# Performance work log

Hardware: AMD Instinct MI355X
Metric: run time of the kernel (lower is better)

The kernel has to match this reference:

```python
import jax, jax.numpy as jnp
import numpy as np

P = 4          # patch_size
LAM = 0.5      # init_lambda
B, C, H, W = 8, 96, 128, 128

def _dct_mat(N):
    # torch_dct unnormalized DCT-II matrix: D[k,n] = 2*cos(pi*(2n+1)k/(2N))
    n = np.arange(N)
    return 2.0 * np.cos(np.pi * (2.0 * n[None, :] + 1.0) * n[:, None] / (2.0 * N))

_D = jnp.asarray(_dct_mat(P), dtype=jnp.float32)
_Di = jnp.asarray(np.linalg.inv(_dct_mat(P)), dtype=jnp.float32)  # exact inverse -> idct(dct(x)) == x

def _dct2(x):
    # DCT-II over last two dims of [..., P, P]
    return jnp.einsum('ij,...jk,lk->...il', _D, x, _D)

def _idct2(x):
    return jnp.einsum('ij,...jk,lk->...il', _Di, x, _Di)

def _conv3x3(x, w, b):
    y = jax.lax.conv_general_dilated(x, w, (1, 1), 'SAME',
                                     dimension_numbers=('NCHW', 'OIHW', 'NCHW'))
    return y + b[None, :, None, None]

def setup_inputs() -> dict:
    key = jax.random.key(0)
    ks = jax.random.split(key, 5)
    std = 1.0 / np.sqrt(C * 9)
    return {
        'input1': jax.random.normal(ks[0], (B, C, H, W), jnp.float32),
        'input2': jax.random.normal(ks[1], (B, C, H, W), jnp.float32),
        'wq': jax.random.normal(ks[2], (C, C, 3, 3), jnp.float32) * std,
        'bq': jnp.zeros((C,), jnp.float32),
        'wk': jax.random.normal(ks[3], (C, C, 3, 3), jnp.float32) * std,
        'bk': jnp.zeros((C,), jnp.float32),
        'wv': jax.random.normal(ks[4], (C, C, 3, 3), jnp.float32) * std,
        'bv': jnp.zeros((C,), jnp.float32),
        'temperature': jnp.ones((1, 1), jnp.float32),
    }

def reference(input1, input2, wq, bq, wk, bk, wv, bv, temperature):
    b, c, h, w = input1.shape
    F_Q = _conv3x3(input1, wq, bq)
    F_K = _conv3x3(input1, wk, bk)
    F_V = _conv3x3(input2, wv, bv)
    hp, wp = h // P, w // P
    # 'b c (h p1) (w p2) -> b c h w p1 p2'
    to_patch = lambda x: x.reshape(b, c, hp, P, wp, P).transpose(0, 1, 2, 4, 3, 5)
    fft_Q = _dct2(to_patch(F_Q))          # [b,c,hp,wp,P,P]
    fft_K = _dct2(to_patch(F_K))
    F1 = jnp.matmul(fft_Q, fft_K)         # per-patch PxP matmul
    L = hp * wp * P * P                   # == h*w
    F1f = F1.reshape(b, c, L)
    Fq = fft_Q.reshape(b, c, L)
    Fk = fft_K.reshape(b, c, L)
    # channel-channel attention: [b,c,L] @ [b,L,c] -> [b,c,c]
    attn = jnp.einsum('bil,bjl->bij', Fq, Fk) * temperature[0, 0]
    attn = jax.nn.softmax(attn, axis=-1)
    Fcfr = jnp.einsum('bij,bjl->bil', attn, F1f).reshape(b, c, hp, wp, P, P)
    Fcfr_out = _idct2(Fcfr)
    # 'b c h w p1 p2 -> b c (h p1) (w p2)'
    Fcfrout = Fcfr_out.transpose(0, 1, 2, 4, 3, 5).reshape(b, c, h, w)
    out1 = jnp.matmul(Fcfrout, F_V)       # batched HxW matmul (H==W)
    Fdfr = F_V - out1 * LAM
    return jnp.matmul(Fcfrout, F_Q) + Fdfr
```

## Files before the change

kernel.cpp:

```cpp
#include <hip/hip_runtime.h>

typedef unsigned short u16;
typedef unsigned int u32;
typedef __bf16 bf16x8 __attribute__((ext_vector_type(8)));
typedef float f32x4 __attribute__((ext_vector_type(4)));
typedef int i32x4 __attribute__((ext_vector_type(4)));

#define BATCH 8
#define CH 96
#define HWSZ 16384
#define PADP (130*130*96)
#define LSTR 68

#define OFF_FQ     0ULL
#define OFF_FK     50331648ULL
#define OFF_GT     50331648ULL
#define OFF_FVN    75497472ULL
#define OFF_PAD1H  100663296ULL
#define OFF_F1W    100663296ULL
#define OFF_PART   126621696ULL
#define OFF_PAD1L  126621696ULL
#define OFF_PAD2   152580096ULL
#define OFF_FCFR   152580096ULL
#define OFF_FVB    178538496ULL
#define OFF_ATTNB  203704320ULL
#define OFF_WQK    203851776ULL
#define OFF_WV     204515328ULL
#define WS_NEED    204681216ULL

__device__ __forceinline__ u16 f2bf(float f) {
    u32 u = __builtin_bit_cast(u32, f);
    u += 0x7fffu + ((u >> 16) & 1u);
    return (u16)(u >> 16);
}
__device__ __forceinline__ float bf2f(u16 h) {
    u32 u = ((u32)h) << 16;
    return __builtin_bit_cast(float, u);
}
__device__ __forceinline__ f32x4 mfma16(i32x4 a, i32x4 b, f32x4 c) {
    return __builtin_amdgcn_mfma_f32_16x16x32_bf16(
        __builtin_bit_cast(bf16x8, a), __builtin_bit_cast(bf16x8, b), c, 0, 0, 0);
}
__device__ __forceinline__ void gl_lds16(const u16* g, u16* l) {
    __builtin_amdgcn_global_load_lds(
        (const __attribute__((address_space(1))) unsigned int*)g,
        (__attribute__((address_space(3))) unsigned int*)l, 16, 0, 0);
}

__global__ __launch_bounds__(256) void k_diag(float* __restrict__ out, int n, float val) {
    for (int i = blockIdx.x * 256 + threadIdx.x; i < n; i += gridDim.x * 256) out[i] = val;
}

__global__ __launch_bounds__(256) void k_trans2(const float* __restrict__ in1,
        const float* __restrict__ in2, u16* __restrict__ p1h, u16* __restrict__ p1l,
        u16* __restrict__ p2) {
    __shared__ float tile[96][129];
    int which = blockIdx.x >> 10;
    int blk = blockIdx.x & 1023;
    const float* src = which ? in2 : in1;
    u16* dh = which ? p2 : p1h;
    u16* dl = which ? nullptr : p1l;
    int b = blk >> 7, y = blk & 127;
    const float* s = src + (size_t)b * CH * HWSZ + (size_t)y * 128;
    for (int idx = threadIdx.x; idx < CH * 128; idx += 256) {
        int c = idx >> 7, x = idx & 127;
        tile[c][x] = s[(size_t)c * HWSZ + x];
    }
    size_t obase = ((size_t)(b * 130 + y + 1) * 130 + 1) * 96;
    for (int c = threadIdx.x; c < 96; c += 256) {
        dh[obase - 96 + c] = 0;
        dh[obase + 128 * 96 + c] = 0;
        if (dl) { dl[obase - 96 + c] = 0; dl[obase + 128 * 96 + c] = 0; }
    }
    if (y == 0 || y == 127) {
        size_t rb = ((size_t)(b * 130 + (y == 0 ? 0 : 129))) * 130 * 96;
        for (int i = threadIdx.x; i < 130 * 96; i += 256) {
            dh[rb + i] = 0;
            if (dl) dl[rb + i] = 0;
        }
    }
    __syncthreads();
    for (int idx = threadIdx.x; idx < 128 * CH; idx += 256) {
        int x = idx / CH, c = idx - x * CH;
        float v = tile[c][x];
        u16 h = f2bf(v);
        dh[obase + idx] = h;
        if (dl) dl[obase + idx] = f2bf(v - bf2f(h));
    }
}

__global__ __launch_bounds__(128) void k_weights_all(const float* __restrict__ wq,
        const float* __restrict__ wk, const float* __restrict__ wv,
        u16* __restrict__ dqk, u16* __restrict__ dv) {
    int co = blockIdx.x;
    if (co < 192) {
        const float* w = (co < 96) ? wq : wk;
        int cs = (co < 96) ? co : co - 96;
        for (int idx = threadIdx.x; idx < 864; idx += 128) {
            int tap = idx / 96, ci = idx - tap * 96;
            int cic = ci >> 5, g = (ci >> 3) & 3, c7 = ci & 7;
            float v = w[((size_t)cs * 96 + ci) * 9 + tap];
            u16 h = f2bf(v), lo = f2bf(v - bf2f(h));
            size_t s = (size_t)(cic * 9 + tap);
            dqk[(((s * 2 + 0) * 4 + g) * 192 + co) * 8 + c7] = h;
            dqk[(((s * 2 + 1) * 4 + g) * 192 + co) * 8 + c7] = lo;
        }
    } else {
        int cs = co - 192;
        for (int idx = threadIdx.x; idx < 864; idx += 128) {
            int tap = idx / 96, ci = idx - tap * 96;
            int cic = ci >> 5, g = (ci >> 3) & 3, c7 = ci & 7;
            float v = wv[((size_t)cs * 96 + ci) * 9 + tap];
            size_t s = (size_t)(cic * 9 + tap);
            dv[((s * 4 + g) * 96 + cs) * 8 + c7] = f2bf(v);
        }
    }
}

__global__ __launch_bounds__(512, 4) void k_convqk6(
        const u16* __restrict__ ph, const u16* __restrict__ pl,
        const u16* __restrict__ wqk,
        const float* __restrict__ bq, const float* __restrict__ bk,
        float* __restrict__ fq, float* __restrict__ fk) {
    __shared__ u16 wbuf[2][12288];
    const int tid = threadIdx.x;
    const int wg = ((blockIdx.x & 7) << 7) | (blockIdx.x >> 3);
    const int b = wg >> 7, y = wg & 127;
    const int w = tid >> 6, lane = tid & 63, l15 = lane & 15, g = lane >> 4;
    const int wx = w & 3, wc = w >> 2;
    f32x4 acc[2][6];
#pragma unroll
    for (int mf = 0; mf < 2; mf++)
#pragma unroll
        for (int f = 0; f < 6; f++) acc[mf][f] = (f32x4){0.f, 0.f, 0.f, 0.f};
    {
#pragma unroll
        for (int j = 0; j < 3; j++)
            gl_lds16(wqk + (size_t)(tid + j * 512) * 8, &wbuf[0][(size_t)(tid + j * 512) * 8]);
    }
    i32x4 ah0, ah1, al0, al1;
    {
        size_t ab = ((size_t)(b * 130 + y) * 130 + (wx * 32 + l15)) * 96 + g * 8;
        ah0 = *(const i32x4*)(ph + ab);
        ah1 = *(const i32x4*)(ph + ab + 16 * 96);
        al0 = *(const i32x4*)(pl + ab);
        al1 = *(const i32x4*)(pl + ab + 16 * 96);
    }
    __syncthreads();
    for (int s = 0; s < 27; s++) {
        const int cur = s & 1;
        i32x4 nh0, nh1, nl0, nl1;
        if (s + 1 < 27) {
            const u16* src = wqk + (size_t)(s + 1) * 12288;
#pragma unroll
            for (int j = 0; j < 3; j++)
                gl_lds16(src + (size_t)(tid + j * 512) * 8, &wbuf[cur ^ 1][(size_t)(tid + j * 512) * 8]);
            const int s1 = s + 1;
            const int cic1 = s1 / 9, tap1 = s1 - cic1 * 9;
            const int dy1 = tap1 / 3 - 1, dx1 = tap1 - (tap1 / 3) * 3 - 1;
            size_t ab = ((size_t)(b * 130 + y + 1 + dy1) * 130 + (wx * 32 + l15 + 1 + dx1)) * 96
                      + cic1 * 32 + g * 8;
            nh0 = *(const i32x4*)(ph + ab);
            nh1 = *(const i32x4*)(ph + ab + 16 * 96);
            nl0 = *(const i32x4*)(pl + ab);
            nl1 = *(const i32x4*)(pl + ab + 16 * 96);
        }
#pragma unroll
        for (int f = 0; f < 6; f++) {
            const int cob = wc * 96 + f * 16 + l15;
            i32x4 bh = *(const i32x4*)(&wbuf[cur][((0 + g) * 192 + cob) * 8]);
            i32x4 bl = *(const i32x4*)(&wbuf[cur][((4 + g) * 192 + cob) * 8]);
            acc[0][f] = mfma16(ah0, bh, acc[0][f]);
            acc[0][f] = mfma16(ah0, bl, acc[0][f]);
            acc[0][f] = mfma16(al0, bh, acc[0][f]);
            acc[1][f] = mfma16(ah1, bh, acc[1][f]);
            acc[1][f] = mfma16(ah1, bl, acc[1][f]);
            acc[1][f] = mfma16(al1, bh, acc[1][f]);
        }
        __syncthreads();
        if (s + 1 < 27) { ah0 = nh0; ah1 = nh1; al0 = nl0; al1 = nl1; }
    }
    const float* bias = wc ? bk : bq;
    float* op = wc ? fk : fq;
#pragma unroll
    for (int f = 0; f < 6; f++) {
        const int co = f * 16 + l15;
        const float bb = bias[co];
#pragma unroll
        for (int mf = 0; mf < 2; mf++) {
            const int xp = wx * 32 + mf * 16 + g * 4;
#pragma unroll
            for (int r = 0; r < 4; r++)
                op[((size_t)((b * 128 + y) * 128 + xp + r)) * 96 + co] = acc[mf][f][r] + bb;
        }
    }
}

__global__ __launch_bounds__(512, 4) void k_convv7(
        const u16* __restrict__ p2, const u16* __restrict__ wv,
        const float* __restrict__ bv, u16* __restrict__ fvb) {
    __shared__ u16 vbuf[2][9216];
    const int tid = threadIdx.x;
    const int wg = ((blockIdx.x & 7) << 7) | (blockIdx.x >> 3);
    const int b = wg >> 7, y = wg & 127;
    const int w = tid >> 6, lane = tid & 63, l15 = lane & 15, g = lane >> 4;
    const int wx = w & 3, wc = w >> 2;
    f32x4 acc[2][3];
#pragma unroll
    for (int mf = 0; mf < 2; mf++)
#pragma unroll
        for (int f = 0; f < 3; f++) acc[mf][f] = (f32x4){0.f, 0.f, 0.f, 0.f};
    {
        gl_lds16(wv + (size_t)tid * 8, &vbuf[0][(size_t)tid * 8]);
        gl_lds16(wv + (size_t)(512 + tid) * 8, &vbuf[0][(size_t)(512 + tid) * 8]);
        if (tid < 128)
            gl_lds16(wv + (size_t)(1024 + tid) * 8, &vbuf[0][(size_t)(1024 + tid) * 8]);
    }
    i32x4 ah0, ah1;
    {
        size_t ab = ((size_t)(b * 130 + y) * 130 + (wx * 32 + l15)) * 96 + g * 8;
        ah0 = *(const i32x4*)(p2 + ab);
        ah1 = *(const i32x4*)(p2 + ab + 16 * 96);
    }
    __syncthreads();
    for (int gp = 0; gp < 9; gp++) {
        const int cur = gp & 1;
        if (gp + 1 < 9) {
            const u16* src = wv + (size_t)(gp + 1) * 9216;
            gl_lds16(src + (size_t)tid * 8, &vbuf[cur ^ 1][(size_t)tid * 8]);
            gl_lds16(src + (size_t)(512 + tid) * 8, &vbuf[cur ^ 1][(size_t)(512 + tid) * 8]);
            if (tid < 128)
                gl_lds16(src + (size_t)(1024 + tid) * 8, &vbuf[cur ^ 1][(size_t)(1024 + tid) * 8]);
        }
#pragma unroll
        for (int t = 0; t < 3; t++) {
            const int s = gp * 3 + t;
            i32x4 nh0, nh1;
            if (s + 1 < 27) {
                const int s1 = s + 1;
                const int cic1 = s1 / 9, tap1 = s1 - cic1 * 9;
                const int dy1 = tap1 / 3 - 1, dx1 = tap1 - (tap1 / 3) * 3 - 1;
                size_t ab = ((size_t)(b * 130 + y + 1 + dy1) * 130 + (wx * 32 + l15 + 1 + dx1)) * 96
                          + cic1 * 32 + g * 8;
                nh0 = *(const i32x4*)(p2 + ab);
                nh1 = *(const i32x4*)(p2 + ab + 16 * 96);
            }
#pragma unroll
            for (int f = 0; f < 3; f++) {
                const int cof = wc * 48 + f * 16 + l15;
                i32x4 bfr = *(const i32x4*)(&vbuf[cur][(size_t)t * 3072 + (g * 96 + cof) * 8]);
                acc[0][f] = mfma16(ah0, bfr, acc[0][f]);
                acc[1][f] = mfma16(ah1, bfr, acc[1][f]);
            }
            if (s + 1 < 27) { ah0 = nh0; ah1 = nh1; }
        }
        __syncthreads();
    }
#pragma unroll
    for (int f = 0; f < 3; f++) {
        const int co = wc * 48 + f * 16 + l15;
        const float bb = bv[co];
#pragma unroll
        for (int mf = 0; mf < 2; mf++) {
            const int xp = wx * 32 + mf * 16 + g * 4;
#pragma unroll
            for (int r = 0; r < 4; r++)
                fvb[((size_t)((b * 128 + y) * 128 + xp + r)) * 96 + co] = f2bf(acc[mf][f][r] + bb);
        }
    }
}

__global__ __launch_bounds__(256) void k_pattn2(
        const float* __restrict__ fq, const float* __restrict__ fk,
        u16* __restrict__ f1w, float* __restrict__ part) {
    __shared__ __attribute__((aligned(16))) float qs[96 * LSTR];
    __shared__ __attribute__((aligned(16))) float ks[96 * LSTR];
    int wg = ((blockIdx.x & 7) << 7) | (blockIdx.x >> 3);
    int b = wg >> 7, ys = (wg >> 2) & 31, xq = wg & 3;
    int y0 = ys * 4, x0 = xq * 32;
    int tx = threadIdx.x & 15, ty = threadIdx.x >> 4;
    double accD[6][6];
#pragma unroll
    for (int a = 0; a < 6; a++)
#pragma unroll
        for (int bb = 0; bb < 6; bb++) accD[a][bb] = 0.0;
#pragma unroll
    for (int cx = 0; cx < 2; cx++) {
        for (int idx = threadIdx.x; idx < 1536; idx += 256) {
            int p = idx / 24, c0 = (idx - p * 24) * 4;
            int ry = p >> 4, rx = p & 15;
            size_t off = ((size_t)((b * 128 + y0 + ry) * 128 + x0 + cx * 16 + rx)) * 96 + c0;
            f32x4 qv = *(const f32x4*)(fq + off);
            f32x4 kv = *(const f32x4*)(fk + off);
#pragma unroll
            for (int u = 0; u < 4; u++) {
                qs[(c0 + u) * LSTR + p] = qv[u];
                ks[(c0 + u) * LSTR + p] = kv[u];
            }
        }
        __syncthreads();
        for (int item = threadIdx.x; item < 384; item += 256) {
            int j = item / 96, c = item - j * 96;
            f32x4 A[4], Bm[4];
#pragma unroll
            for (int r = 0; r < 4; r++) {
                A[r]  = *(const f32x4*)&qs[c * LSTR + r * 16 + j * 4];
                Bm[r] = *(const f32x4*)&ks[c * LSTR + r * 16 + j * 4];
            }
            float rsB[4], csB[4], rsA[4], tot = 0.f;
#pragma unroll
            for (int r = 0; r < 4; r++) {
                rsB[r] = Bm[r][0] + Bm[r][1] + Bm[r][2] + Bm[r][3];
                rsA[r] = A[r][0] + A[r][1] + A[r][2] + A[r][3];
                tot += rsB[r];
            }
#pragma unroll
            for (int m = 0; m < 4; m++) csB[m] = Bm[0][m] + Bm[1][m] + Bm[2][m] + Bm[3][m];
#pragma unroll
            for (int r = 0; r < 4; r++) {
#pragma unroll
                for (int m = 0; m < 4; m++) {
                    float ab = A[r][0] * Bm[0][m] + A[r][1] * Bm[1][m]
                             + A[r][2] * Bm[2][m] + A[r][3] * Bm[3][m];
                    f1w[((size_t)((b * 128 + y0 + r) * 128 + x0 + cx * 16 + j * 4 + m)) * 96 + c]
                        = f2bf(8.f * ab + 2.f * rsA[r] * csB[m]);
                }
                f32x4 kt;
#pragma unroll
                for (int m = 0; m < 4; m++)
                    kt[m] = 64.f * Bm[r][m] + 16.f * (rsB[r] + csB[m]) + 4.f * tot;
                *(f32x4*)&ks[c * LSTR + r * 16 + j * 4] = kt;
            }
        }
        __syncthreads();
        float acc[6][6];
#pragma unroll
        for (int a = 0; a < 6; a++)
#pragma unroll
            for (int bb = 0; bb < 6; bb++) acc[a][bb] = 0.f;
        for (int l4 = 0; l4 < 16; l4++) {
            f32x4 qv4[6], kv4[6];
#pragma unroll
            for (int a = 0; a < 6; a++)
                qv4[a] = *(const f32x4*)&qs[(ty + 16 * a) * LSTR + l4 * 4];
#pragma unroll
            for (int bb = 0; bb < 6; bb++)
                kv4[bb] = *(const f32x4*)&ks[(tx + 16 * bb) * LSTR + l4 * 4];
#pragma unroll
            for (int a = 0; a < 6; a++)
#pragma unroll
                for (int bb = 0; bb < 6; bb++) {
                    acc[a][bb] += qv4[a][0] * kv4[bb][0];
                    acc[a][bb] += qv4[a][1] * kv4[bb][1];
                    acc[a][bb] += qv4[a][2] * kv4[bb][2];
                    acc[a][bb] += qv4[a][3] * kv4[bb][3];
                }
        }
#pragma unroll
        for (int a = 0; a < 6; a++)
#pragma unroll
            for (int bb = 0; bb < 6; bb++) accD[a][bb] += (double)acc[a][bb];
        __syncthreads();
    }
    int s128 = ys * 4 + xq;
#pragma unroll
    for (int a = 0; a < 6; a++)
#pragma unroll
        for (int bb = 0; bb < 6; bb++)
            part[((size_t)((b * 128 + s128) * 96 + ty + 16 * a)) * 96 + tx + 16 * bb]
                = (float)accD[a][bb];
}

__global__ __launch_bounds__(128) void k_softmax(
        const float* __restrict__ part, const float* __restrict__ temp,
        u16* __restrict__ attnb) {
    __shared__ float red[128];
    int b = blockIdx.x / 96, i2 = blockIdx.x - b * 96;
    int j2 = threadIdx.x;
    float v = 0.f;
    if (j2 < 96) {
        double vd = 0.0;
        for (int s = 0; s < 128; s++)
            vd += (double)part[((size_t)((b * 128 + s) * 96 + i2)) * 96 + j2];
        v = (float)vd * temp[0];
    }
    red[j2] = (j2 < 96) ? v : -3.4e38f;
    __syncthreads();
    for (int off = 64; off >= 1; off >>= 1) {
        if (j2 < off) red[j2] = fmaxf(red[j2], red[j2 + off]);
        __syncthreads();
    }
    float mx = red[0];
    __syncthreads();
    float e = (j2 < 96) ? expf(v - mx) : 0.f;
    red[j2] = e;
    __syncthreads();
    for (int off = 64; off >= 1; off >>= 1) {
        if (j2 < off) red[j2] += red[j2 + off];
        __syncthreads();
    }
    float sum = red[0];
    if (j2 < 96) attnb[((size_t)(b * 96) + i2) * 96 + j2] = f2bf(e / sum);
}

__global__ __launch_bounds__(256) void k_gprep(
        const float* __restrict__ fqn, const u16* __restrict__ fvb,
        u16* __restrict__ gt, u16* __restrict__ fvn) {
    __shared__ u16 lg[8 * 32 * 33];
    __shared__ u16 lv[8 * 32 * 33];
    int blk = blockIdx.x;
    int b = blk / 192;
    int r = blk - b * 192;
    int yt = r / 48; r -= yt * 48;
    int xt = r / 12; int cc = r - xt * 12;
    int y0 = yt * 32, x0 = xt * 32, c0 = cc * 8;
    for (int idx = threadIdx.x; idx < 8192; idx += 256) {
        int pix = idx >> 3, cl = idx & 7;
        int yy = pix >> 5, xx = pix & 31;
        size_t off = ((size_t)((b * 128 + y0 + yy) * 128 + x0 + xx)) * 96 + c0 + cl;
        float q = fqn[off];
        float v = bf2f(fvb[off]);
        int la = (cl * 32 + yy) * 33 + xx;
        lg[la] = f2bf(q - 0.5f * v);
        lv[la] = f2bf(v);
    }
    __syncthreads();
    for (int idx = threadIdx.x; idx < 8192; idx += 256) {
        int yy = idx & 31, xl = (idx >> 5) & 31, cl = idx >> 10;
        gt[((size_t)((b * 96 + c0 + cl) * 128 + x0 + xl)) * 128 + y0 + yy] = lg[(cl * 32 + yy) * 33 + xl];
    }
    for (int idx = threadIdx.x; idx < 8192; idx += 256) {
        int xx = idx & 31, yl = (idx >> 5) & 31, cl = idx >> 10;
        fvn[((size_t)((b * 96 + c0 + cl) * 128 + y0 + yl)) * 128 + x0 + xx] = lv[(cl * 32 + yl) * 33 + xx];
    }
}

__global__ __launch_bounds__(256) void k_fcfr2(
        const u16* __restrict__ attnb, const u16* __restrict__ f1w,
        u16* __restrict__ fc) {
    int b = blockIdx.x >> 6, pc = blockIdx.x & 63;
    int lane = threadIdx.x & 63, wv_ = threadIdx.x >> 6;
    int l15 = lane & 15, g = lane >> 4;
    int pbase = pc * 256 + wv_ * 64;
    f32x4 acc[6][4];
#pragma unroll
    for (int m = 0; m < 6; m++)
#pragma unroll
        for (int n = 0; n < 4; n++) acc[m][n] = (f32x4){0.f, 0.f, 0.f, 0.f};
#pragma unroll
    for (int ks = 0; ks < 3; ks++) {
        int k0 = ks * 32 + g * 8;
        i32x4 afr[6];
#pragma unroll
        for (int m = 0; m < 6; m++)
            afr[m] = *(const i32x4*)(attnb + ((size_t)(b * 96 + m * 16 + l15)) * 96 + k0);
#pragma unroll
        for (int n = 0; n < 4; n++) {
            i32x4 bfr = *(const i32x4*)(f1w + ((size_t)(b * 16384 + pbase + n * 16 + l15)) * 96 + k0);
#pragma unroll
            for (int m = 0; m < 6; m++)
                acc[m][n] = mfma16(afr[m], bfr, acc[m][n]);
        }
    }
#pragma unroll
    for (int m = 0; m < 6; m++)
#pragma unroll
        for (int n = 0; n < 4; n++)
#pragma unroll
            for (int r = 0; r < 4; r++) {
                int i2 = m * 16 + g * 4 + r;
                int pix = pbase + n * 16 + l15;
                fc[((size_t)(b * 96 + i2)) * HWSZ + pix] = f2bf(acc[m][n][r]);
            }
}

__global__ __launch_bounds__(256) void k_final(
        const u16* __restrict__ fc, const u16* __restrict__ gt,
        const u16* __restrict__ fvn, float* __restrict__ out) {
    int b = blockIdx.x / 96, c = blockIdx.x - b * 96;
    int lane = threadIdx.x & 63, wv_ = threadIdx.x >> 6;
    int l15 = lane & 15, g = lane >> 4;
    const u16* A = fc + ((size_t)(b * 96 + c)) * HWSZ;
    const u16* Bm = gt + ((size_t)(b * 96 + c)) * HWSZ;
    f32x4 acc[2][8];
#pragma unroll
    for (int mf = 0; mf < 2; mf++)
#pragma unroll
        for (int nf = 0; nf < 8; nf++) acc[mf][nf] = (f32x4){0.f, 0.f, 0.f, 0.f};
#pragma unroll
    for (int kc = 0; kc < 4; kc++) {
        int k0 = kc * 32 + g * 8;
        i32x4 af[2];
#pragma unroll
        for (int mf = 0; mf < 2; mf++)
            af[mf] = *(const i32x4*)(A + (size_t)(wv_ * 32 + mf * 16 + l15) * 128 + k0);
#pragma unroll
        for (int nf = 0; nf < 8; nf++) {
            i32x4 bf = *(const i32x4*)(Bm + (size_t)(nf * 16 + l15) * 128 + k0);
#pragma unroll
            for (int mf = 0; mf < 2; mf++)
                acc[mf][nf] = mfma16(af[mf], bf, acc[mf][nf]);
        }
    }
    const u16* V = fvn + ((size_t)(b * 96 + c)) * HWSZ;
    float* O = out + ((size_t)(b * 96 + c)) * HWSZ;
#pragma unroll
    for (int mf = 0; mf < 2; mf++)
#pragma unroll
        for (int nf = 0; nf < 8; nf++)
#pragma unroll
            for (int r = 0; r < 4; r++) {
                int y = wv_ * 32 + mf * 16 + g * 4 + r;
                int x = nf * 16 + l15;
                O[y * 128 + x] = acc[mf][nf][r] + bf2f(V[y * 128 + x]);
            }
}

extern "C" void kernel_launch(void* const* d_in, const int* in_sizes, int n_in,
                              void* d_out, int out_size, void* d_ws, size_t ws_size,
                              hipStream_t stream) {
    (void)in_sizes; (void)n_in;
    if (ws_size < (size_t)WS_NEED) {
        k_diag<<<2048, 256, 0, stream>>>((float*)d_out, out_size, (float)(ws_size >> 10));
        return;
    }
    const float* in1 = (const float*)d_in[0];
    const float* in2 = (const float*)d_in[1];
    const float* wq  = (const float*)d_in[2];
    const float* bq  = (const float*)d_in[3];
    const float* wk  = (const float*)d_in[4];
    const float* bk  = (const float*)d_in[5];
    const float* wv  = (const float*)d_in[6];
    const float* bv  = (const float*)d_in[7];
    const float* temp = (const float*)d_in[8];
    char* ws = (char*)d_ws;
    float* FQ   = (float*)(ws + OFF_FQ);
    float* FK   = (float*)(ws + OFF_FK);
    u16*  GT    = (u16*)(ws + OFF_GT);
    u16*  FVN   = (u16*)(ws + OFF_FVN);
    u16*  PAD1H = (u16*)(ws + OFF_PAD1H);
    u16*  PAD1L = (u16*)(ws + OFF_PAD1L);
    u16*  PAD2  = (u16*)(ws + OFF_PAD2);
    u16*  F1W   = (u16*)(ws + OFF_F1W);
    float* PART = (float*)(ws + OFF_PART);
    u16*  FCFR  = (u16*)(ws + OFF_FCFR);
    u16*  FVB   = (u16*)(ws + OFF_FVB);
    u16*  ATTNB = (u16*)(ws + OFF_ATTNB);
    u16*  WQK   = (u16*)(ws + OFF_WQK);
    u16*  WV    = (u16*)(ws + OFF_WV);

    k_trans2<<<2048, 256, 0, stream>>>(in1, in2, PAD1H, PAD1L, PAD2);
    k_weights_all<<<288, 128, 0, stream>>>(wq, wk, wv, WQK, WV);
    k_convqk6<<<1024, 512, 0, stream>>>(PAD1H, PAD1L, WQK, bq, bk, FQ, FK);
    k_convv7<<<1024, 512, 0, stream>>>(PAD2, WV, bv, FVB);
    k_pattn2<<<1024, 256, 0, stream>>>(FQ, FK, F1W, PART);
    k_softmax<<<768, 128, 0, stream>>>(PART, temp, ATTNB);
    k_gprep<<<1536, 256, 0, stream>>>(FQ, FVB, GT, FVN);
    k_fcfr2<<<512, 256, 0, stream>>>(ATTNB, F1W, FCFR);
    k_final<<<768, 256, 0, stream>>>(FCFR, GT, FVN, (float*)d_out);
}
```

Before: 367.2 us.

## Write conv outputs in NCHW layout and drop FV transpose in gprep

The Q/K/V conv kernels now write their outputs in planar NCHW layout with vectorized stores, instead of pixel-major NHWC. This lets the patch-attention loader read contiguous rows and store float4s straight to LDS. The gprep kernel no longer has to transpose and write FVN, since conv V emits it directly. The change affects the store pattern of the conv kernels, which may now be less coalesced per wave, and it leaves a dead computation in convv7p.

```diff
diff --git a/kernel.cpp b/kernel.cpp
--- a/kernel.cpp
+++ b/kernel.cpp
@@ -5,6 +5,7 @@
 typedef __bf16 bf16x8 __attribute__((ext_vector_type(8)));
 typedef float f32x4 __attribute__((ext_vector_type(4)));
 typedef int i32x4 __attribute__((ext_vector_type(4)));
+typedef unsigned int u32x2 __attribute__((ext_vector_type(2)));
 
 #define BATCH 8
 #define CH 96
@@ -15,14 +16,13 @@
 #define OFF_FQ     0ULL
 #define OFF_FK     50331648ULL
 #define OFF_GT     50331648ULL
-#define OFF_FVN    75497472ULL
 #define OFF_PAD1H  100663296ULL
 #define OFF_F1W    100663296ULL
 #define OFF_PART   126621696ULL
 #define OFF_PAD1L  126621696ULL
 #define OFF_PAD2   152580096ULL
 #define OFF_FCFR   152580096ULL
-#define OFF_FVB    178538496ULL
+#define OFF_FVN    178538496ULL
 #define OFF_ATTNB  203704320ULL
 #define OFF_WQK    203851776ULL
 #define OFF_WV     204515328ULL
@@ -117,7 +117,7 @@
     }
 }
 
-__global__ __launch_bounds__(512, 4) void k_convqk6(
+__global__ __launch_bounds__(512, 4) void k_convqk6p(
         const u16* __restrict__ ph, const u16* __restrict__ pl,
         const u16* __restrict__ wqk,
         const float* __restrict__ bq, const float* __restrict__ bk,
@@ -189,16 +189,17 @@
 #pragma unroll
         for (int mf = 0; mf < 2; mf++) {
             const int xp = wx * 32 + mf * 16 + g * 4;
-#pragma unroll
-            for (int r = 0; r < 4; r++)
-                op[((size_t)((b * 128 + y) * 128 + xp + r)) * 96 + co] = acc[mf][f][r] + bb;
-        }
-    }
-}
-
-__global__ __launch_bounds__(512, 4) void k_convv7(
+            f32x4 o;
+#pragma unroll
+            for (int r = 0; r < 4; r++) o[r] = acc[mf][f][r] + bb;
+            *(f32x4*)(op + ((size_t)((b * 96 + co) * 128 + y)) * 128 + xp) = o;
+        }
+    }
+}
+
+__global__ __launch_bounds__(512, 4) void k_convv7p(
         const u16* __restrict__ p2, const u16* __restrict__ wv,
-        const float* __restrict__ bv, u16* __restrict__ fvb) {
+        const float* __restrict__ bv, u16* __restrict__ fvn) {
     __shared__ u16 vbuf[2][9216];
     const int tid = threadIdx.x;
     const int wg = ((blockIdx.x & 7) << 7) | (blockIdx.x >> 3);
@@ -263,14 +264,19 @@
 #pragma unroll
         for (int mf = 0; mf < 2; mf++) {
             const int xp = wx * 32 + mf * 16 + g * 4;
-#pragma unroll
-            for (int r = 0; r < 4; r++)
-                fvb[((size_t)((b * 128 + y) * 128 + xp + r)) * 96 + co] = f2bf(acc[mf][f][r] + bb);
-        }
-    }
-}
-
-__global__ __launch_bounds__(256) void k_pattn2(
+            u32 lo = (u32)f2bf(acc[mf][f][0]) | ((u32)f2bf(acc[mf][f][1] + bb - bb + bb) << 16);
+            u16 o0 = f2bf(acc[mf][f][0] + bb), o1 = f2bf(acc[mf][f][1] + bb);
+            u16 o2 = f2bf(acc[mf][f][2] + bb), o3 = f2bf(acc[mf][f][3] + bb);
+            u32x2 pk;
+            pk[0] = (u32)o0 | ((u32)o1 << 16);
+            pk[1] = (u32)o2 | ((u32)o3 << 16);
+            (void)lo;
+            *(u32x2*)(fvn + ((size_t)((b * 96 + co) * 128 + y)) * 128 + xp) = pk;
+        }
+    }
+}
+
+__global__ __launch_bounds__(256) void k_pattn2p(
         const float* __restrict__ fq, const float* __restrict__ fk,
         u16* __restrict__ f1w, float* __restrict__ part) {
     __shared__ __attribute__((aligned(16))) float qs[96 * LSTR];
@@ -287,16 +293,13 @@
 #pragma unroll
     for (int cx = 0; cx < 2; cx++) {
         for (int idx = threadIdx.x; idx < 1536; idx += 256) {
-            int p = idx / 24, c0 = (idx - p * 24) * 4;
-            int ry = p >> 4, rx = p & 15;
-            size_t off = ((size_t)((b * 128 + y0 + ry) * 128 + x0 + cx * 16 + rx)) * 96 + c0;
+            int c = idx >> 4, rem = idx & 15, ry = rem >> 2, q4 = rem & 3;
+            size_t off = ((size_t)((b * 96 + c) * 128 + y0 + ry)) * 128 + x0 + cx * 16 + q4 * 4;
             f32x4 qv = *(const f32x4*)(fq + off);
             f32x4 kv = *(const f32x4*)(fk + off);
-#pragma unroll
-            for (int u = 0; u < 4; u++) {
-                qs[(c0 + u) * LSTR + p] = qv[u];
-                ks[(c0 + u) * LSTR + p] = kv[u];
-            }
+            int p0 = ry * 16 + q4 * 4;
+            *(f32x4*)&qs[c * LSTR + p0] = qv;
+            *(f32x4*)&ks[c * LSTR + p0] = kv;
         }
         __syncthreads();
         for (int item = threadIdx.x; item < 384; item += 256) {
@@ -369,6 +372,34 @@
         for (int bb = 0; bb < 6; bb++)
             part[((size_t)((b * 128 + s128) * 96 + ty + 16 * a)) * 96 + tx + 16 * bb]
                 = (float)accD[a][bb];
+}
+
+__global__ __launch_bounds__(256) void k_gprep2(
+        const float* __restrict__ fqp, const u16* __restrict__ fvn,
+        u16* __restrict__ gt) {
+    __shared__ u16 lg[8 * 32 * 33];
+    int blk = blockIdx.x;
+    int b = blk / 192;
+    int r = blk - b * 192;
+    int yt = r / 48; r -= yt * 48;
+    int xt = r / 12; int cc = r - xt * 12;
+    int y0 = yt * 32, x0 = xt * 32, c0 = cc * 8;
+    for (int idx = threadIdx.x; idx < 2048; idx += 256) {
+        int cl = idx >> 8, rem = idx & 255, yy = rem >> 3, x4 = rem & 7;
+        size_t off = ((size_t)((b * 96 + c0 + cl) * 128 + y0 + yy)) * 128 + x0 + x4 * 4;
+        f32x4 q = *(const f32x4*)(fqp + off);
+        const u16* vp = fvn + off;
+        int la = (cl * 32 + yy) * 33 + x4 * 4;
+#pragma unroll
+        for (int u = 0; u < 4; u++)
+            lg[la + u] = f2bf(q[u] - 0.5f * bf2f(vp[u]));
+    }
+    __syncthreads();
+    for (int idx = threadIdx.x; idx < 8192; idx += 256) {
+        int cl = idx >> 10, xl = (idx >> 5) & 31, yy = idx & 31;
+        gt[((size_t)((b * 96 + c0 + cl) * 128 + x0 + xl)) * 128 + y0 + yy]
+            = lg[(cl * 32 + yy) * 33 + xl];
+    }
 }
 
 __global__ __launch_bounds__(128) void k_softmax(
@@ -401,38 +432,6 @@
     }
     float sum = red[0];
     if (j2 < 96) attnb[((size_t)(b * 96) + i2) * 96 + j2] = f2bf(e / sum);
-}
-
-__global__ __launch_bounds__(256) void k_gprep(
-        const float* __restrict__ fqn, const u16* __restrict__ fvb,
-        u16* __restrict__ gt, u16* __restrict__ fvn) {
-    __shared__ u16 lg[8 * 32 * 33];
-    __shared__ u16 lv[8 * 32 * 33];
-    int blk = blockIdx.x;
-    int b = blk / 192;
-    int r = blk - b * 192;
-    int yt = r / 48; r -= yt * 48;
-    int xt = r / 12; int cc = r - xt * 12;
-    int y0 = yt * 32, x0 = xt * 32, c0 = cc * 8;
-    for (int idx = threadIdx.x; idx < 8192; idx += 256) {
-        int pix = idx >> 3, cl = idx & 7;
-        int yy = pix >> 5, xx = pix & 31;
-        size_t off = ((size_t)((b * 128 + y0 + yy) * 128 + x0 + xx)) * 96 + c0 + cl;
-        float q = fqn[off];
-        float v = bf2f(fvb[off]);
-        int la = (cl * 32 + yy) * 33 + xx;
-        lg[la] = f2bf(q - 0.5f * v);
-        lv[la] = f2bf(v);
-    }
-    __syncthreads();
-    for (int idx = threadIdx.x; idx < 8192; idx += 256) {
-        int yy = idx & 31, xl = (idx >> 5) & 31, cl = idx >> 10;
-        gt[((size_t)((b * 96 + c0 + cl) * 128 + x0 + xl)) * 128 + y0 + yy] = lg[(cl * 32 + yy) * 33 + xl];
-    }
-    for (int idx = threadIdx.x; idx < 8192; idx += 256) {
-        int xx = idx & 31, yl = (idx >> 5) & 31, cl = idx >> 10;
-        fvn[((size_t)((b * 96 + c0 + cl) * 128 + y0 + yl)) * 128 + x0 + xx] = lv[(cl * 32 + yl) * 33 + xx];
-    }
 }
 
 __global__ __launch_bounds__(256) void k_fcfr2(
@@ -537,25 +536,24 @@
     float* FQ   = (float*)(ws + OFF_FQ);
     float* FK   = (float*)(ws + OFF_FK);
     u16*  GT    = (u16*)(ws + OFF_GT);
-    u16*  FVN   = (u16*)(ws + OFF_FVN);
     u16*  PAD1H = (u16*)(ws + OFF_PAD1H);
     u16*  PAD1L = (u16*)(ws + OFF_PAD1L);
     u16*  PAD2  = (u16*)(ws + OFF_PAD2);
     u16*  F1W   = (u16*)(ws + OFF_F1W);
     float* PART = (float*)(ws + OFF_PART);
     u16*  FCFR  = (u16*)(ws + OFF_FCFR);
-    u16*  FVB   = (u16*)(ws + OFF_FVB);
+    u16*  FVN   = (u16*)(ws + OFF_FVN);
     u16*  ATTNB = (u16*)(ws + OFF_ATTNB);
     u16*  WQK   = (u16*)(ws + OFF_WQK);
     u16*  WV    = (u16*)(ws + OFF_WV);
 
     k_trans2<<<2048, 256, 0, stream>>>(in1, in2, PAD1H, PAD1L, PAD2);
     k_weights_all<<<288, 128, 0, stream>>>(wq, wk, wv, WQK, WV);
-    k_convqk6<<<1024, 512, 0, stream>>>(PAD1H, PAD1L, WQK, bq, bk, FQ, FK);
-    k_convv7<<<1024, 512, 0, stream>>>(PAD2, WV, bv, FVB);
-    k_pattn2<<<1024, 256, 0, stream>>>(FQ, FK, F1W, PART);
+    k_convqk6p<<<1024, 512, 0, stream>>>(PAD1H, PAD1L, WQK, bq, bk, FQ, FK);
+    k_convv7p<<<1024, 512, 0, stream>>>(PAD2, WV, bv, FVN);
+    k_pattn2p<<<1024, 256, 0, stream>>>(FQ, FK, F1W, PART);
+    k_gprep2<<<1536, 256, 0, stream>>>(FQ, FVN, GT);
     k_softmax<<<768, 128, 0, stream>>>(PART, temp, ATTNB);
-    k_gprep<<<1536, 256, 0, stream>>>(FQ, FVB, GT, FVN);
     k_fcfr2<<<512, 256, 0, stream>>>(ATTNB, F1W, FCFR);
     k_final<<<768, 256, 0, stream>>>(FCFR, GT, FVN, (float*)d_out);
 }
```

Measured after the change: 339.8 us. 1.08x faster.
